# Kernel tuning notes

Hardware: AMD Instinct MI355X
Metric: run time of the kernel (lower is better)

Reference implementation:

```python
import jax, jax.numpy as jnp
import numpy as np

HEAD_DIM = 128
N_HEADS = 32
N_KV_HEADS = 8
EPS = 1e-6
ROPE_THETA = 1e6
NEG_INF = -1e9


def _rms_norm(x, w):
    # per-head RMSNorm over last dim (head_dim), fp32 math like Qwen3RMSNorm
    xf = x.astype(jnp.float32)
    var = jnp.mean(xf * xf, axis=-1, keepdims=True)
    return (w * (xf * jax.lax.rsqrt(var + EPS))).astype(x.dtype)


def _rope_cos_sin(position_ids, dtype):
    # default rope: inv_freq = theta^(-2i/d), emb = cat(freqs, freqs)
    inv_freq = 1.0 / (ROPE_THETA ** (jnp.arange(0, HEAD_DIM, 2, dtype=jnp.float32) / HEAD_DIM))
    freqs = position_ids.astype(jnp.float32)[:, :, None] * inv_freq[None, None, :]  # [B,S,hd/2]
    emb = jnp.concatenate([freqs, freqs], axis=-1)  # [B,S,hd]
    return jnp.cos(emb).astype(dtype), jnp.sin(emb).astype(dtype)


def _rotate_half(x):
    x1, x2 = jnp.split(x, 2, axis=-1)
    return jnp.concatenate([-x2, x1], axis=-1)


def setup_inputs() -> dict:
    key = jax.random.key(0)
    ks = jax.random.split(key, 6)
    B, S, H = 1, 2048, 4096
    return {
        "hidden_states": jax.random.normal(ks[0], (B, S, H), jnp.float32),
        "position_ids": jnp.broadcast_to(jnp.arange(S, dtype=jnp.int32)[None, :], (B, S)),
        "Wq": jax.random.normal(ks[1], (N_HEADS * HEAD_DIM, H), jnp.float32) * 0.02,
        "Wk": jax.random.normal(ks[2], (N_KV_HEADS * HEAD_DIM, H), jnp.float32) * 0.02,
        "Wv": jax.random.normal(ks[3], (N_KV_HEADS * HEAD_DIM, H), jnp.float32) * 0.02,
        "Wo": jax.random.normal(ks[4], (H, N_HEADS * HEAD_DIM), jnp.float32) * 0.02,
        "q_norm_w": jnp.ones((HEAD_DIM,), jnp.float32),
        "k_norm_w": jnp.ones((HEAD_DIM,), jnp.float32),
    }


def reference(hidden_states, position_ids, Wq, Wk, Wv, Wo, q_norm_w, k_norm_w):
    B, S, H = hidden_states.shape
    scaling = HEAD_DIM ** -0.5
    n_rep = N_HEADS // N_KV_HEADS

    # projections (torch Linear: y = x @ W.T), reshape to [B, heads, S, hd]
    q = jnp.einsum('bsh,dh->bsd', hidden_states, Wq).reshape(B, S, N_HEADS, HEAD_DIM)
    k = jnp.einsum('bsh,dh->bsd', hidden_states, Wk).reshape(B, S, N_KV_HEADS, HEAD_DIM)
    v = jnp.einsum('bsh,dh->bsd', hidden_states, Wv).reshape(B, S, N_KV_HEADS, HEAD_DIM)

    q = _rms_norm(q, q_norm_w).transpose(0, 2, 1, 3)  # [B,nH,S,hd]
    k = _rms_norm(k, k_norm_w).transpose(0, 2, 1, 3)  # [B,nKV,S,hd]
    v = v.transpose(0, 2, 1, 3)

    cos, sin = _rope_cos_sin(position_ids, hidden_states.dtype)
    cos = cos[:, None, :, :]  # unsqueeze head dim
    sin = sin[:, None, :, :]
    q = q * cos + _rotate_half(q) * sin
    k = k * cos + _rotate_half(k) * sin

    # GQA repeat_kv
    k = jnp.repeat(k, n_rep, axis=1)
    v = jnp.repeat(v, n_rep, axis=1)

    scores = jnp.einsum('bhqd,bhkd->bhqk', q, k) * scaling
    causal = jnp.where(
        jnp.arange(S)[:, None] >= jnp.arange(S)[None, :], 0.0, NEG_INF
    ).astype(scores.dtype)
    scores = scores + causal[None, None, :, :]
    attn = jax.nn.softmax(scores.astype(jnp.float32), axis=-1).astype(q.dtype)

    out = jnp.einsum('bhqk,bhkd->bhqd', attn, v)
    out = out.transpose(0, 2, 1, 3).reshape(B, S, N_HEADS * HEAD_DIM)
    return jnp.einsum('bsd,hd->bsh', out, Wo)
```

## Files before the change

### kernel.cpp

```cpp
#include <hip/hip_runtime.h>
#include <hip/hip_bf16.h>

typedef unsigned short u16;
typedef __bf16 bf16x8 __attribute__((ext_vector_type(8)));
typedef u16 u16x4 __attribute__((ext_vector_type(4)));
typedef u16 u16x8 __attribute__((ext_vector_type(8)));
typedef float f32x4 __attribute__((ext_vector_type(4)));

#define S_LEN  2048
#define HID    4096
#define NHEADS 32
#define NKV    8
#define HD     128
#define QDIM   (NHEADS*HD)
#define KVDIM  (NKV*HD)
#define NT     (S_LEN/64)

__device__ __forceinline__ u16 f2bf(float f) {
  unsigned u = __float_as_uint(f);
  u += 0x7fff + ((u >> 16) & 1);
  return (u16)(u >> 16);
}
__device__ __forceinline__ void lds_load16(const u16* g, u16* l) {
  __builtin_amdgcn_global_load_lds(
      (__attribute__((address_space(1))) void*)(g),
      (__attribute__((address_space(3))) void*)(l), 16, 0, 0);
}

__global__ __launch_bounds__(256) void f2b4(
    const float* __restrict__ s0, u16* __restrict__ d0, long n0,
    const float* __restrict__ s1, u16* __restrict__ d1, long n1,
    const float* __restrict__ s2, u16* __restrict__ d2, long n2,
    const float* __restrict__ s3, u16* __restrict__ d3, long n3)
{
  const float* s; u16* d; long n; int b0, nb;
  const int b = blockIdx.x;
  if (b < 1024)      { s=s0; d=d0; n=n0; b0=0;    nb=1024; }
  else if (b < 3072) { s=s1; d=d1; n=n1; b0=1024; nb=2048; }
  else if (b < 3584) { s=s2; d=d2; n=n2; b0=3072; nb=512;  }
  else               { s=s3; d=d3; n=n3; b0=3584; nb=512;  }
  long i = (long)(b - b0)*256 + threadIdx.x;
  const long stride = (long)nb*256;
  for (; i < n; i += stride) {
    f32x4 a = ((const f32x4*)s)[i*2];
    f32x4 c = ((const f32x4*)s)[i*2 + 1];
    u16x8 o;
    #pragma unroll
    for (int j = 0; j < 4; ++j) { o[j] = f2bf(a[j]); o[4+j] = f2bf(c[j]); }
    ((u16x8*)d)[i] = o;
  }
}

__global__ __launch_bounds__(256) void f2b(
    const float* __restrict__ in, u16* __restrict__ out, long n8)
{
  long i = (long)blockIdx.x * blockDim.x + threadIdx.x;
  const long stride = (long)gridDim.x * blockDim.x;
  for (; i < n8; i += stride) {
    f32x4 a = ((const f32x4*)in)[i*2];
    f32x4 b = ((const f32x4*)in)[i*2 + 1];
    u16x8 o;
    #pragma unroll
    for (int j = 0; j < 4; ++j) { o[j] = f2bf(a[j]); o[4+j] = f2bf(b[j]); }
    ((u16x8*)out)[i] = o;
  }
}

template<int CMODE>
__global__ __launch_bounds__(512, 2) void gemm8(
    const u16* __restrict__ A, const u16* __restrict__ B,
    void* __restrict__ Cq, void* __restrict__ Ck, void* __restrict__ Cv,
    int M, int N, int K)
{
  __shared__ u16 lds[65536];
  const int tid  = threadIdx.x;
  const int lane = tid & 63;
  const int w    = tid >> 6;
  const int wr   = w >> 2, wc = w & 3;
  const int l16  = lane & 15, lhi = lane >> 4;
  const long arow0 = (long)blockIdx.y * 256;
  const long brow0 = (long)blockIdx.x * 256;
  const int ntiles = K >> 6;

  const u16* Ag[2]; const u16* Bg[2];
  #pragma unroll
  for (int r = 0; r < 2; ++r) {
    const int p  = r*4096 + w*512 + lane*8;
    const int lr = p >> 6;
    const int cu = (p & 63) ^ ((lr & 7) << 3);
    Ag[r] = A + (arow0 + (lr >> 6)*128 + (lr & 63))*(long)K + cu;
    Bg[r] = B + (brow0 + (lr >> 5)*64  + (lr & 31))*(long)K + cu;
  }
  u16* const dstA = lds + w*512;
  u16* const dstB = lds + 32768 + w*512;

  auto stageA = [&](int s, int kt) {
    const long so = (long)(kt*64) + (long)(s*64)*K;
    u16* d = dstA + (((kt & 1)*2 + s) << 13);
    lds_load16(Ag[0] + so, d);
    lds_load16(Ag[1] + so, d + 4096);
  };
  auto stageB = [&](int s, int kt) {
    const long so = (long)(kt*64) + (long)(s*32)*K;
    u16* d = dstB + (((kt & 1)*2 + s) << 13);
    lds_load16(Bg[0] + so, d);
    lds_load16(Bg[1] + so, d + 4096);
  };

  const int xr = (l16 & 7) << 3;
  int offA[4][2], offB[2][2];
  #pragma unroll
  for (int m2 = 0; m2 < 4; ++m2)
    #pragma unroll
    for (int ks = 0; ks < 2; ++ks)
      offA[m2][ks] = (wr*64 + m2*16 + l16)*64 + ((ks*32 + lhi*8) ^ xr);
  #pragma unroll
  for (int n2 = 0; n2 < 2; ++n2)
    #pragma unroll
    for (int ks = 0; ks < 2; ++ks)
      offB[n2][ks] = (wc*32 + n2*16 + l16)*64 + ((ks*32 + lhi*8) ^ xr);

  f32x4 acc[8][4] = {};

  stageA(0, 0); stageB(0, 0); stageB(1, 0); stageA(1, 0);
  stageA(0, 1); stageB(0, 1); stageB(1, 1);
  asm volatile("s_waitcnt vmcnt(6)" ::: "memory");
  __builtin_amdgcn_s_barrier();

  #pragma unroll 2
  for (int t = 0; t < ntiles; ++t) {
    const int Ab = (t & 1) << 14;
    const int Bb = 32768 + ((t & 1) << 14);
    bf16x8 af[4][2], bf[2][2], af2[4][2], bf2[2][2];

    #pragma unroll
    for (int m2 = 0; m2 < 4; ++m2)
      #pragma unroll
      for (int ks = 0; ks < 2; ++ks)
        af[m2][ks] = *(const bf16x8*)(lds + Ab + offA[m2][ks]);
    #pragma unroll
    for (int n2 = 0; n2 < 2; ++n2)
      #pragma unroll
      for (int ks = 0; ks < 2; ++ks)
        bf[n2][ks] = *(const bf16x8*)(lds + Bb + offB[n2][ks]);
    if (t + 1 < ntiles) stageA(1, t + 1);
    __builtin_amdgcn_s_barrier();
    asm volatile("s_waitcnt lgkmcnt(0)" ::: "memory");
    __builtin_amdgcn_s_setprio(1);
    #pragma unroll
    for (int m2 = 0; m2 < 4; ++m2)
      #pragma unroll
      for (int n2 = 0; n2 < 2; ++n2)
        #pragma unroll
        for (int ks = 0; ks < 2; ++ks)
          acc[m2][n2] = __builtin_amdgcn_mfma_f32_16x16x32_bf16(
              af[m2][ks], bf[n2][ks], acc[m2][n2], 0, 0, 0);
    __builtin_amdgcn_s_setprio(0);
    __builtin_amdgcn_s_barrier();

    #pragma unroll
    for (int n2 = 0; n2 < 2; ++n2)
      #pragma unroll
      for (int ks = 0; ks < 2; ++ks)
        bf2[n2][ks] = *(const bf16x8*)(lds + Bb + 8192 + offB[n2][ks]);
    if (t + 2 < ntiles) stageA(0, t + 2);
    __builtin_amdgcn_s_barrier();
    asm volatile("s_waitcnt lgkmcnt(0)" ::: "memory");
    __builtin_amdgcn_s_setprio(1);
    #pragma unroll
    for (int m2 = 0; m2 < 4; ++m2)
      #pragma unroll
      for (int n2 = 0; n2 < 2; ++n2)
        #pragma unroll
        for (int ks = 0; ks < 2; ++ks)
          acc[m2][2+n2] = __builtin_amdgcn_mfma_f32_16x16x32_bf16(
              af[m2][ks], bf2[n2][ks], acc[m2][2+n2], 0, 0, 0);
    __builtin_amdgcn_s_setprio(0);
    __builtin_amdgcn_s_barrier();

    #pragma unroll
    for (int m2 = 0; m2 < 4; ++m2)
      #pragma unroll
      for (int ks = 0; ks < 2; ++ks)
        af2[m2][ks] = *(const bf16x8*)(lds + Ab + 8192 + offA[m2][ks]);
    if (t + 2 < ntiles) stageB(0, t + 2);
    __builtin_amdgcn_s_barrier();
    asm volatile("s_waitcnt lgkmcnt(0)" ::: "memory");
    __builtin_amdgcn_s_setprio(1);
    #pragma unroll
    for (int m2 = 0; m2 < 4; ++m2)
      #pragma unroll
      for (int n2 = 0; n2 < 2; ++n2)
        #pragma unroll
        for (int ks = 0; ks < 2; ++ks)
          acc[4+m2][2+n2] = __builtin_amdgcn_mfma_f32_16x16x32_bf16(
              af2[m2][ks], bf2[n2][ks], acc[4+m2][2+n2], 0, 0, 0);
    __builtin_amdgcn_s_setprio(0);
    __builtin_amdgcn_s_barrier();

    if (t + 2 < ntiles) stageB(1, t + 2);
    __builtin_amdgcn_s_barrier();
    __builtin_amdgcn_s_setprio(1);
    #pragma unroll
    for (int m2 = 0; m2 < 4; ++m2)
      #pragma unroll
      for (int n2 = 0; n2 < 2; ++n2)
        #pragma unroll
        for (int ks = 0; ks < 2; ++ks)
          acc[4+m2][n2] = __builtin_amdgcn_mfma_f32_16x16x32_bf16(
              af2[m2][ks], bf[n2][ks], acc[4+m2][n2], 0, 0, 0);
    __builtin_amdgcn_s_setprio(0);
    if (t + 2 < ntiles) { asm volatile("s_waitcnt vmcnt(6)" ::: "memory"); }
    else                { asm volatile("s_waitcnt vmcnt(0)" ::: "memory"); }
    __builtin_amdgcn_s_barrier();
  }

  #pragma unroll
  for (int m = 0; m < 8; ++m) {
    const long row = arow0 + wr*128 + m*16 + lhi*4;
    #pragma unroll
    for (int n = 0; n < 4; ++n) {
      const long col = brow0 + wc*64 + n*16 + l16;
      if (CMODE == 1) {
        #pragma unroll
        for (int r = 0; r < 4; ++r)
          ((float*)Cq)[(row + r)*N + col] = acc[m][n][r];
      } else {
        if (blockIdx.x < 16) {
          #pragma unroll
          for (int r = 0; r < 4; ++r)
            ((u16*)Cq)[(row + r)*QDIM + col] = f2bf(acc[m][n][r]);
        } else if (blockIdx.x < 20) {
          #pragma unroll
          for (int r = 0; r < 4; ++r)
            ((u16*)Ck)[(row + r)*KVDIM + (col - QDIM)] = f2bf(acc[m][n][r]);
        } else {
          u16x4 o;
          #pragma unroll
          for (int r = 0; r < 4; ++r) o[r] = f2bf(acc[m][n][r]);
          *(u16x4*)((u16*)Cv + (col - QDIM - KVDIM)*(long)S_LEN + row) = o;
        }
      }
    }
  }
}

__global__ __launch_bounds__(256) void norm_rope2(
    u16* __restrict__ Qb, u16* __restrict__ Kb,
    const float* __restrict__ qw, const float* __restrict__ kw,
    const int* __restrict__ pos)
{
  const int row  = blockIdx.x * 4 + (threadIdx.x >> 6);
  const int lane = threadIdx.x & 63;
  u16* p; const float* nw; float sc; int s;
  if (row < S_LEN*NHEADS) {
    p = Qb + (long)row * HD; nw = qw; sc = 0.08838834764831845f; s = row >> 5;
  } else {
    const int r2 = row - S_LEN*NHEADS;
    p = Kb + (long)r2 * HD; nw = kw; sc = 1.0f; s = r2 >> 3;
  }

  float x1 = __uint_as_float(((unsigned)p[lane]) << 16);
  float x2 = __uint_as_float(((unsigned)p[lane + 64]) << 16);
  float ss = x1*x1 + x2*x2;
  #pragma unroll
  for (int m = 32; m >= 1; m >>= 1) ss += __shfl_xor(ss, m);
  const float inv = rsqrtf(ss * (1.0f/128.0f) + 1e-6f);
  x1 *= inv * nw[lane];
  x2 *= inv * nw[lane + 64];

  const float inv_freq = expf(-(float)lane * (13.815510557964274f / 64.0f));
  const float ang = (float)pos[s] * inv_freq;
  float sn, cs;
  sincosf(ang, &sn, &cs);
  p[lane]      = f2bf((x1*cs - x2*sn) * sc);
  p[lane + 64] = f2bf((x2*cs + x1*sn) * sc);
}

__global__ __launch_bounds__(256, 4) void attn(
    const u16* __restrict__ Q, const u16* __restrict__ K,
    const u16* __restrict__ VT, u16* __restrict__ O)
{
  __shared__ u16 Ks[64*128];
  __shared__ u16 Vt[128*64];
  __shared__ u16 Ps[4*16*64];

  const int tid  = threadIdx.x;
  const int lane = tid & 63;
  const int w    = tid >> 6;
  const int l16  = lane & 15, lhi = lane >> 4;
  const int h    = blockIdx.y;
  const int kh   = h >> 2;
  const int T    = (NT - 1) - ((blockIdx.x + blockIdx.y) & (NT - 1));
  const int qrow0 = T*64 + w*16;

  bf16x8 qf[4];
  #pragma unroll
  for (int ks = 0; ks < 4; ++ks)
    qf[ks] = *(const bf16x8*)(Q + (long)(qrow0 + l16)*QDIM + h*HD + ks*32 + lhi*8);

  float mr[4] = {-1e30f,-1e30f,-1e30f,-1e30f};
  float lr[4] = {0.f,0.f,0.f,0.f};
  f32x4 of[8] = {};
  u16* Pw = Ps + w*16*64;

  for (int t = 0; t <= T; ++t) {
    const int kv0 = t * 64;
    #pragma unroll
    for (int i = 0; i < 4; ++i) {
      const int r   = w*16 + i*4 + lhi;
      const int col = (l16*8) ^ ((r & 7) << 3);
      lds_load16(K + (long)(kv0 + r)*KVDIM + kh*HD + col,
                 Ks + (w*16 + i*4)*128);
    }
    #pragma unroll
    for (int i = 0; i < 4; ++i) {
      const int r   = w*32 + i*8 + (lane >> 3);
      const int col = ((lane & 7)*8) ^ ((r & 7) << 3);
      lds_load16(VT + (long)(kh*HD + r)*S_LEN + kv0 + col,
                 Vt + (w*32 + i*8)*64);
    }
    __syncthreads();

    f32x4 sa[4] = {};
    __builtin_amdgcn_s_setprio(1);
    #pragma unroll
    for (int n = 0; n < 4; ++n)
      #pragma unroll
      for (int ks = 0; ks < 4; ++ks) {
        bf16x8 kf = *(const bf16x8*)(
            Ks + (n*16 + l16)*128 + ((ks*32 + lhi*8) ^ ((l16 & 7) << 3)));
        sa[n] = __builtin_amdgcn_mfma_f32_16x16x32_bf16(qf[ks], kf, sa[n], 0, 0, 0);
      }
    __builtin_amdgcn_s_setprio(0);

    const bool diag = (t == T);
    float pm[4];
    #pragma unroll
    for (int r = 0; r < 4; ++r) {
      const int grow = qrow0 + lhi*4 + r;
      #pragma unroll
      for (int n = 0; n < 4; ++n) {
        float sv = sa[n][r];
        if (diag && (kv0 + n*16 + l16 > grow)) sv = -1e9f;
        sa[n][r] = sv;
      }
      float p01 = fmaxf(sa[0][r], sa[1][r]);
      float p23 = fmaxf(sa[2][r], sa[3][r]);
      float pmx = fmaxf(p01, p23);
      pmx = fmaxf(pmx, __shfl_xor(pmx, 1));
      pmx = fmaxf(pmx, __shfl_xor(pmx, 2));
      pmx = fmaxf(pmx, __shfl_xor(pmx, 4));
      pmx = fmaxf(pmx, __shfl_xor(pmx, 8));
      pm[r] = pmx;
    }
    bool need = (pm[0] > mr[0] + 8.f) | (pm[1] > mr[1] + 8.f) |
                (pm[2] > mr[2] + 8.f) | (pm[3] > mr[3] + 8.f);
    if (__any(need)) {
      #pragma unroll
      for (int r = 0; r < 4; ++r) {
        const float mnew  = fmaxf(mr[r], pm[r]);
        const float alpha = __expf(mr[r] - mnew);
        mr[r] = mnew;
        lr[r] *= alpha;
        #pragma unroll
        for (int c = 0; c < 8; ++c) of[c][r] *= alpha;
      }
    }
    #pragma unroll
    for (int r = 0; r < 4; ++r) {
      float rsum = 0.f;
      #pragma unroll
      for (int n = 0; n < 4; ++n) {
        float pv = __expf(sa[n][r] - mr[r]);
        sa[n][r] = pv;
        rsum += pv;
      }
      rsum += __shfl_xor(rsum, 1);
      rsum += __shfl_xor(rsum, 2);
      rsum += __shfl_xor(rsum, 4);
      rsum += __shfl_xor(rsum, 8);
      lr[r] += rsum;
    }

    #pragma unroll
    for (int r = 0; r < 4; ++r) {
      const int prow = lhi*4 + r;
      #pragma unroll
      for (int n = 0; n < 4; ++n)
        Pw[prow*64 + ((n*16 + l16) ^ ((prow & 7) << 3))] = f2bf(sa[n][r]);
    }
    __builtin_amdgcn_s_setprio(1);
    #pragma unroll
    for (int ks = 0; ks < 2; ++ks) {
      bf16x8 pf = *(const bf16x8*)(
          Pw + l16*64 + ((ks*32 + lhi*8) ^ ((l16 & 7) << 3)));
      #pragma unroll
      for (int c = 0; c < 8; ++c) {
        bf16x8 vf = *(const bf16x8*)(
            Vt + (c*16 + l16)*64 + ((ks*32 + lhi*8) ^ ((l16 & 7) << 3)));
        of[c] = __builtin_amdgcn_mfma_f32_16x16x32_bf16(pf, vf, of[c], 0, 0, 0);
      }
    }
    __builtin_amdgcn_s_setprio(0);
    __syncthreads();
  }

  #pragma unroll
  for (int r = 0; r < 4; ++r) {
    const float invl = 1.0f / lr[r];
    const long orow = (long)(qrow0 + lhi*4 + r) * QDIM + h*HD;
    #pragma unroll
    for (int c = 0; c < 8; ++c)
      O[orow + c*16 + l16] = f2bf(of[c][r] * invl);
  }
}

extern "C" void kernel_launch(void* const* d_in, const int* in_sizes, int n_in,
                              void* d_out, int out_size, void* d_ws, size_t ws_size,
                              hipStream_t stream) {
  (void)in_sizes; (void)n_in; (void)out_size; (void)ws_size;
  const float* hs  = (const float*)d_in[0];
  const int*   pos = (const int*)d_in[1];
  const float* Wq  = (const float*)d_in[2];
  const float* Wk  = (const float*)d_in[3];
  const float* Wv  = (const float*)d_in[4];
  const float* Wo  = (const float*)d_in[5];
  const float* qw  = (const float*)d_in[6];
  const float* kw  = (const float*)d_in[7];

  u16* hsB = (u16*)d_ws;
  u16* W1  = hsB + (long)S_LEN*HID;
  u16* WkB = W1  + (long)QDIM*HID;
  u16* WvB = WkB + (long)KVDIM*HID;
  u16* Kb  = WvB + (long)KVDIM*HID;
  u16* VT  = Kb  + (long)S_LEN*KVDIM;
  u16* AO  = VT  + (long)KVDIM*S_LEN;
  u16* Qb  = (u16*)d_out;

  f2b4<<<4096, 256, 0, stream>>>(hs, hsB, (long)S_LEN*HID/8,
                                 Wq, W1,  (long)QDIM*HID/8,
                                 Wk, WkB, (long)KVDIM*HID/8,
                                 Wv, WvB, (long)KVDIM*HID/8);

  gemm8<3><<<dim3((QDIM+2*KVDIM)/256, S_LEN/256), 512, 0, stream>>>(
      hsB, W1, Qb, Kb, VT, S_LEN, QDIM+2*KVDIM, HID);

  norm_rope2<<<(S_LEN*NHEADS + S_LEN*NKV)/4, 256, 0, stream>>>(
      Qb, Kb, qw, kw, pos);

  f2b<<<2048, 256, 0, stream>>>(Wo, W1, (long)HID*QDIM/8);

  attn<<<dim3(NT, NHEADS), 256, 0, stream>>>(Qb, Kb, VT, AO);

  gemm8<1><<<dim3(HID/256, S_LEN/256), 512, 0, stream>>>(
      AO, W1, d_out, nullptr, nullptr, S_LEN, HID, QDIM);
}
```

Measured before the change: 408.6 us.

## Double-buffer K/V tiles in attention and add a 128x256 fp32-output GEMM

The attention kernel now double-buffers the K and V tiles in LDS. The next tile's K is prefetched after QK^T and V after PV, with split vmcnt waits replacing full syncthreads. This hides global-to-LDS latency but doubles LDS use, so occupancy drops to 2 blocks per CU. The output projection switches to a new gemmF kernel with 128x256 tiles and a pipelined quarter-tile MFMA schedule that writes fp32 directly, giving more blocks to cover the CUs.

```diff
diff --git a/kernel.cpp b/kernel.cpp
--- a/kernel.cpp
+++ b/kernel.cpp
@@ -245,6 +245,162 @@
   }
 }
 
+__global__ __launch_bounds__(512, 2) void gemmF(
+    const u16* __restrict__ A, const u16* __restrict__ B,
+    float* __restrict__ C, int M, int N, int K)
+{
+  __shared__ u16 lds[49152];
+  const int tid  = threadIdx.x;
+  const int lane = tid & 63;
+  const int w    = tid >> 6;
+  const int wr   = w >> 2, wc = w & 3;
+  const int l16  = lane & 15, lhi = lane >> 4;
+  const long arow0 = (long)blockIdx.y * 128;
+  const long brow0 = (long)blockIdx.x * 256;
+  const int ntiles = K >> 6;
+
+  const int cu = ((lane & 7) ^ (lane >> 3)) * 8;
+  const int rA  = (w >> 2)*64 + (w & 3)*8;
+  const int rB1c = 128 + (w >> 2)*64 + (w & 3)*8;
+  const u16* srcA  = A + (arow0 + rA   + (lane >> 3))*(long)K + cu;
+  const u16* srcB0 = B + (brow0 + rA   + (lane >> 3))*(long)K + cu;
+  const u16* srcB1 = B + (brow0 + rB1c + (lane >> 3))*(long)K + cu;
+  u16* const dA  = lds + rA*64;
+  u16* const dB0 = lds + 16384 + rA*64;
+  u16* const dB1 = lds + 16384 + rB1c*64;
+
+  auto stageA = [&](int s, int kt) {
+    lds_load16(srcA + (long)(s*32)*K + kt*64,
+               dA + ((kt & 1) << 13) + s*2048);
+  };
+  auto stageB = [&](int s, int kt) {
+    const long so = (long)(s*32)*K + kt*64;
+    const int  d  = ((kt & 1) << 14) + s*2048;
+    lds_load16(srcB0 + so, dB0 + d);
+    lds_load16(srcB1 + so, dB1 + d);
+  };
+
+  const int xr = (l16 & 7) << 3;
+  int offA[2][2], offB[2][2];
+  #pragma unroll
+  for (int m = 0; m < 2; ++m)
+    #pragma unroll
+    for (int ks = 0; ks < 2; ++ks)
+      offA[m][ks] = (wr*64 + m*16 + l16)*64 + ((ks*32 + lhi*8) ^ xr);
+  #pragma unroll
+  for (int n = 0; n < 2; ++n)
+    #pragma unroll
+    for (int ks = 0; ks < 2; ++ks)
+      offB[n][ks] = (wc*64 + n*16 + l16)*64 + ((ks*32 + lhi*8) ^ xr);
+
+  f32x4 acc[4][4] = {};
+
+  stageA(0, 0); stageA(1, 0); stageB(0, 0); stageB(1, 0);
+  if (ntiles > 1) { stageA(0, 1); stageB(0, 1); stageB(1, 1); }
+  asm volatile("s_waitcnt vmcnt(5)" ::: "memory");
+  __builtin_amdgcn_s_barrier();
+
+  #pragma unroll 2
+  for (int t = 0; t < ntiles; ++t) {
+    const int Ab = (t & 1) << 13;
+    const int Bb = 16384 + ((t & 1) << 14);
+    bf16x8 af[2][2], bf[2][2], af2[2][2], bf2[2][2];
+
+    #pragma unroll
+    for (int m = 0; m < 2; ++m)
+      #pragma unroll
+      for (int ks = 0; ks < 2; ++ks)
+        af[m][ks] = *(const bf16x8*)(lds + Ab + offA[m][ks]);
+    #pragma unroll
+    for (int n = 0; n < 2; ++n)
+      #pragma unroll
+      for (int ks = 0; ks < 2; ++ks)
+        bf[n][ks] = *(const bf16x8*)(lds + Bb + offB[n][ks]);
+    if (t + 1 < ntiles) stageA(1, t + 1);
+    __builtin_amdgcn_s_barrier();
+    asm volatile("s_waitcnt lgkmcnt(0)" ::: "memory");
+    __builtin_amdgcn_s_setprio(1);
+    #pragma unroll
+    for (int m = 0; m < 2; ++m)
+      #pragma unroll
+      for (int n = 0; n < 2; ++n)
+        #pragma unroll
+        for (int ks = 0; ks < 2; ++ks)
+          acc[m][n] = __builtin_amdgcn_mfma_f32_16x16x32_bf16(
+              af[m][ks], bf[n][ks], acc[m][n], 0, 0, 0);
+    __builtin_amdgcn_s_setprio(0);
+    __builtin_amdgcn_s_barrier();
+
+    #pragma unroll
+    for (int n = 0; n < 2; ++n)
+      #pragma unroll
+      for (int ks = 0; ks < 2; ++ks)
+        bf2[n][ks] = *(const bf16x8*)(lds + Bb + 2048 + offB[n][ks]);
+    if (t + 2 < ntiles) stageA(0, t + 2);
+    __builtin_amdgcn_s_barrier();
+    asm volatile("s_waitcnt lgkmcnt(0)" ::: "memory");
+    __builtin_amdgcn_s_setprio(1);
+    #pragma unroll
+    for (int m = 0; m < 2; ++m)
+      #pragma unroll
+      for (int n = 0; n < 2; ++n)
+        #pragma unroll
+        for (int ks = 0; ks < 2; ++ks)
+          acc[m][2+n] = __builtin_amdgcn_mfma_f32_16x16x32_bf16(
+              af[m][ks], bf2[n][ks], acc[m][2+n], 0, 0, 0);
+    __builtin_amdgcn_s_setprio(0);
+    __builtin_amdgcn_s_barrier();
+
+    #pragma unroll
+    for (int m = 0; m < 2; ++m)
+      #pragma unroll
+      for (int ks = 0; ks < 2; ++ks)
+        af2[m][ks] = *(const bf16x8*)(lds + Ab + 2048 + offA[m][ks]);
+    if (t + 2 < ntiles) stageB(0, t + 2);
+    __builtin_amdgcn_s_barrier();
+    asm volatile("s_waitcnt lgkmcnt(0)" ::: "memory");
+    __builtin_amdgcn_s_setprio(1);
+    #pragma unroll
+    for (int m = 0; m < 2; ++m)
+      #pragma unroll
+      for (int n = 0; n < 2; ++n)
+        #pragma unroll
+        for (int ks = 0; ks < 2; ++ks)
+          acc[2+m][2+n] = __builtin_amdgcn_mfma_f32_16x16x32_bf16(
+              af2[m][ks], bf2[n][ks], acc[2+m][2+n], 0, 0, 0);
+    __builtin_amdgcn_s_setprio(0);
+    __builtin_amdgcn_s_barrier();
+
+    if (t + 2 < ntiles) stageB(1, t + 2);
+    __builtin_amdgcn_s_barrier();
+    __builtin_amdgcn_s_setprio(1);
+    #pragma unroll
+    for (int m = 0; m < 2; ++m)
+      #pragma unroll
+      for (int n = 0; n < 2; ++n)
+        #pragma unroll
+        for (int ks = 0; ks < 2; ++ks)
+          acc[2+m][n] = __builtin_amdgcn_mfma_f32_16x16x32_bf16(
+              af2[m][ks], bf[n][ks], acc[2+m][n], 0, 0, 0);
+    __builtin_amdgcn_s_setprio(0);
+    if (t + 2 < ntiles) { asm volatile("s_waitcnt vmcnt(5)" ::: "memory"); }
+    else                { asm volatile("s_waitcnt vmcnt(0)" ::: "memory"); }
+    __builtin_amdgcn_s_barrier();
+  }
+
+  #pragma unroll
+  for (int mi = 0; mi < 4; ++mi) {
+    const long row = arow0 + wr*64 + (mi >> 1)*32 + (mi & 1)*16 + lhi*4;
+    #pragma unroll
+    for (int ni = 0; ni < 4; ++ni) {
+      const long col = brow0 + wc*64 + (ni >> 1)*32 + (ni & 1)*16 + l16;
+      #pragma unroll
+      for (int r = 0; r < 4; ++r)
+        C[(row + r)*N + col] = acc[mi][ni][r];
+    }
+  }
+}
+
 __global__ __launch_bounds__(256) void norm_rope2(
     u16* __restrict__ Qb, u16* __restrict__ Kb,
     const float* __restrict__ qw, const float* __restrict__ kw,
@@ -277,12 +433,12 @@
   p[lane + 64] = f2bf((x2*cs + x1*sn) * sc);
 }
 
-__global__ __launch_bounds__(256, 4) void attn(
+__global__ __launch_bounds__(256, 2) void attn(
     const u16* __restrict__ Q, const u16* __restrict__ K,
     const u16* __restrict__ VT, u16* __restrict__ O)
 {
-  __shared__ u16 Ks[64*128];
-  __shared__ u16 Vt[128*64];
+  __shared__ u16 Ks[2][64*128];
+  __shared__ u16 Vt[2][128*64];
   __shared__ u16 Ps[4*16*64];
 
   const int tid  = threadIdx.x;
@@ -299,28 +455,40 @@
   for (int ks = 0; ks < 4; ++ks)
     qf[ks] = *(const bf16x8*)(Q + (long)(qrow0 + l16)*QDIM + h*HD + ks*32 + lhi*8);
 
+  auto stageK = [&](int buf, int t) {
+    const long kv0 = t * 64;
+    #pragma unroll
+    for (int i = 0; i < 4; ++i) {
+      const int r = w*16 + i*4 + lhi;
+      lds_load16(K + (kv0 + r)*(long)KVDIM + kh*HD + ((l16*8) ^ ((r & 7) << 3)),
+                 &Ks[buf][(w*16 + i*4)*128]);
+    }
+  };
+  auto stageV = [&](int buf, int t) {
+    const long kv0 = t * 64;
+    #pragma unroll
+    for (int i = 0; i < 4; ++i) {
+      const int r = w*32 + i*8 + (lane >> 3);
+      lds_load16(VT + (long)(kh*HD + r)*S_LEN + kv0 + (((lane & 7)*8) ^ ((r & 7) << 3)),
+                 &Vt[buf][(w*32 + i*8)*64]);
+    }
+  };
+
   float mr[4] = {-1e30f,-1e30f,-1e30f,-1e30f};
   float lr[4] = {0.f,0.f,0.f,0.f};
   f32x4 of[8] = {};
   u16* Pw = Ps + w*16*64;
 
+  stageK(0, 0); stageV(0, 0);
+
   for (int t = 0; t <= T; ++t) {
+    const int cur = t & 1;
     const int kv0 = t * 64;
-    #pragma unroll
-    for (int i = 0; i < 4; ++i) {
-      const int r   = w*16 + i*4 + lhi;
-      const int col = (l16*8) ^ ((r & 7) << 3);
-      lds_load16(K + (long)(kv0 + r)*KVDIM + kh*HD + col,
-                 Ks + (w*16 + i*4)*128);
-    }
-    #pragma unroll
-    for (int i = 0; i < 4; ++i) {
-      const int r   = w*32 + i*8 + (lane >> 3);
-      const int col = ((lane & 7)*8) ^ ((r & 7) << 3);
-      lds_load16(VT + (long)(kh*HD + r)*S_LEN + kv0 + col,
-                 Vt + (w*32 + i*8)*64);
-    }
-    __syncthreads();
+    const u16* Kc = Ks[cur];
+    const u16* Vc = Vt[cur];
+
+    asm volatile("s_waitcnt vmcnt(4)" ::: "memory");
+    __builtin_amdgcn_s_barrier();
 
     f32x4 sa[4] = {};
     __builtin_amdgcn_s_setprio(1);
@@ -329,10 +497,11 @@
       #pragma unroll
       for (int ks = 0; ks < 4; ++ks) {
         bf16x8 kf = *(const bf16x8*)(
-            Ks + (n*16 + l16)*128 + ((ks*32 + lhi*8) ^ ((l16 & 7) << 3)));
+            Kc + (n*16 + l16)*128 + ((ks*32 + lhi*8) ^ ((l16 & 7) << 3)));
         sa[n] = __builtin_amdgcn_mfma_f32_16x16x32_bf16(qf[ks], kf, sa[n], 0, 0, 0);
       }
     __builtin_amdgcn_s_setprio(0);
+    if (t < T) stageK(cur ^ 1, t + 1);
 
     const bool diag = (t == T);
     float pm[4];
@@ -390,6 +559,11 @@
       for (int n = 0; n < 4; ++n)
         Pw[prow*64 + ((n*16 + l16) ^ ((prow & 7) << 3))] = f2bf(sa[n][r]);
     }
+
+    if (t < T) { asm volatile("s_waitcnt vmcnt(4)" ::: "memory"); }
+    else       { asm volatile("s_waitcnt vmcnt(0)" ::: "memory"); }
+    __builtin_amdgcn_s_barrier();
+
     __builtin_amdgcn_s_setprio(1);
     #pragma unroll
     for (int ks = 0; ks < 2; ++ks) {
@@ -398,12 +572,12 @@
       #pragma unroll
       for (int c = 0; c < 8; ++c) {
         bf16x8 vf = *(const bf16x8*)(
-            Vt + (c*16 + l16)*64 + ((ks*32 + lhi*8) ^ ((l16 & 7) << 3)));
+            Vc + (c*16 + l16)*64 + ((ks*32 + lhi*8) ^ ((l16 & 7) << 3)));
         of[c] = __builtin_amdgcn_mfma_f32_16x16x32_bf16(pf, vf, of[c], 0, 0, 0);
       }
     }
     __builtin_amdgcn_s_setprio(0);
-    __syncthreads();
+    if (t < T) stageV(cur ^ 1, t + 1);
   }
 
   #pragma unroll
@@ -453,6 +627,6 @@
 
   attn<<<dim3(NT, NHEADS), 256, 0, stream>>>(Qb, Kb, VT, AO);
 
-  gemm8<1><<<dim3(HID/256, S_LEN/256), 512, 0, stream>>>(
-      AO, W1, d_out, nullptr, nullptr, S_LEN, HID, QDIM);
-}
+  gemmF<<<dim3(HID/256, S_LEN/128), 512, 0, stream>>>(
+      AO, W1, (float*)d_out, S_LEN, HID, QDIM);
+}
```

Result: faster. 399.3 us (-2.3%).
